# Optimization experiments

Hardware: AMD Instinct MI355X
Metric: run time of the kernel (lower is better)

Reference implementation:

```python
import jax, jax.numpy as jnp
import numpy as np

D_MODEL = 1024
H = 16
HEAD = D_MODEL // H  # 64


def setup_inputs() -> dict:
    key = jax.random.key(0)
    ks = jax.random.split(key, 10)
    B, S = 2, 2048
    x = jax.random.normal(ks[0], (B, S, D_MODEL), dtype=jnp.float32)
    y = jax.random.normal(ks[1], (B, S, D_MODEL), dtype=jnp.float32)
    mask = jnp.ones((B, S, S), dtype=jnp.float32)
    s = 1.0 / np.sqrt(D_MODEL)
    Wq = jax.random.normal(ks[2], (D_MODEL, D_MODEL), dtype=jnp.float32) * s
    Wk = jax.random.normal(ks[3], (D_MODEL, D_MODEL), dtype=jnp.float32) * s
    Wv = jax.random.normal(ks[4], (D_MODEL, D_MODEL), dtype=jnp.float32) * s
    Wo = jax.random.normal(ks[5], (D_MODEL, D_MODEL), dtype=jnp.float32) * s
    bq = jnp.zeros((D_MODEL,), jnp.float32)
    bk = jnp.zeros((D_MODEL,), jnp.float32)
    bv = jnp.zeros((D_MODEL,), jnp.float32)
    bo = jnp.zeros((D_MODEL,), jnp.float32)
    return {"x": x, "y": y, "mask": mask, "Wq": Wq, "bq": bq, "Wk": Wk,
            "bk": bk, "Wv": Wv, "bv": bv, "Wo": Wo, "bo": bo}


def reference(x, y, mask, Wq, bq, Wk, bk, Wv, bv, Wo, bo):
    # torch Linear: out = in @ W.T + b; here W stored as [out, in]
    B, Sq, D = x.shape
    Skv = y.shape[1]
    q = x @ Wq.T + bq  # [B, Sq, D]
    k = y @ Wk.T + bk  # [B, Skv, D]
    v = y @ Wv.T + bv
    # chunk(h, dim=-1) + cat(dim=0) == split feature dim into heads (head-major)
    q = q.reshape(B, Sq, H, HEAD)
    k = k.reshape(B, Skv, H, HEAD)
    v = v.reshape(B, Skv, H, HEAD)
    score = jnp.einsum('bqhd,bkhd->bhqk', q, k) / np.sqrt(HEAD)
    score = score + (1.0 - mask[:, None, :, :]) * -1e9
    attn = jax.nn.softmax(score, axis=-1)
    out = jnp.einsum('bhqk,bkhd->bqhd', attn, v).reshape(B, Sq, D)
    return out @ Wo.T + bo
```

## Files before the change

### kernel.cpp

```cpp
#include <hip/hip_runtime.h>
#include <cstdint>
#include <cstddef>

typedef __bf16 bf16x8 __attribute__((ext_vector_type(8)));
typedef float f32x4 __attribute__((ext_vector_type(4)));
typedef unsigned short u16;
typedef unsigned short u16x8 __attribute__((ext_vector_type(8)));
typedef unsigned int u32;

typedef __attribute__((address_space(1))) void gvoid_t;
typedef __attribute__((address_space(3))) void lvoid_t;

__device__ __forceinline__ void gld_lds16(const void* g, void* l) {
  __builtin_amdgcn_global_load_lds((gvoid_t*)g, (lvoid_t*)l, 16, 0, 0);
}

__device__ __forceinline__ u16 f2bf(float f) {
  u32 u = __float_as_uint(f);
  u += 0x7fffu + ((u >> 16) & 1u);
  return (u16)(u >> 16);
}
__device__ __forceinline__ u32 pack_rnd(float a, float b) {
  const u32 ua = __float_as_uint(a) + 0x8000u;
  const u32 ub = __float_as_uint(b) + 0x8000u;
  return __builtin_amdgcn_perm(ub, ua, 0x07060302u);
}
__device__ __forceinline__ bf16x8 ld_frag(const u16* p) {
  return __builtin_bit_cast(bf16x8, *(const uint4*)p);
}
__device__ __forceinline__ f32x4 mfma16(bf16x8 a, bf16x8 b, f32x4 c) {
  return __builtin_amdgcn_mfma_f32_16x16x32_bf16(a, b, c, 0, 0, 0);
}
__device__ __forceinline__ float ex2(float x) {
  return __builtin_amdgcn_exp2f(x);
}

#define D_MODEL 1024
#define SEQ     2048
#define NHEAD   16
#define QSC     0.1803368801f
#define MBIAS   (-1.4426950408e9f)

__global__ __launch_bounds__(256) void cvt_kernel(
    const float* __restrict__ x,  const float* __restrict__ y,
    const float* __restrict__ wq, const float* __restrict__ wk,
    const float* __restrict__ wv, const float* __restrict__ wo,
    u16* __restrict__ xb, u16* __restrict__ yb,
    u16* __restrict__ wqb, u16* __restrict__ wkb,
    u16* __restrict__ wvb, u16* __restrict__ wob) {
  const int t = blockIdx.y;
  const float* src;
  u16* dst;
  int n;
  float sc = 1.0f;
  if (t == 0)      { src = x;  dst = xb;  n = 4096 * 1024; }
  else if (t == 1) { src = y;  dst = yb;  n = 4096 * 1024; }
  else if (t == 2) { src = wq; dst = wqb; n = 1024 * 1024; sc = QSC; }
  else if (t == 3) { src = wk; dst = wkb; n = 1024 * 1024; }
  else if (t == 4) { src = wv; dst = wvb; n = 1024 * 1024; }
  else             { src = wo; dst = wob; n = 1024 * 1024; }
  const int i = (blockIdx.x * 256 + threadIdx.x) * 8;
  if (i >= n) return;
  const float4 a = *(const float4*)(src + i);
  const float4 b = *(const float4*)(src + i + 4);
  ushort4 lo, hi;
  lo.x = f2bf(a.x * sc); lo.y = f2bf(a.y * sc); lo.z = f2bf(a.z * sc); lo.w = f2bf(a.w * sc);
  hi.x = f2bf(b.x * sc); hi.y = f2bf(b.y * sc); hi.z = f2bf(b.z * sc); hi.w = f2bf(b.w * sc);
  *(ushort4*)(dst + i) = lo;
  *(ushort4*)(dst + i + 4) = hi;
}

__global__ __launch_bounds__(256) void maskC_kernel(
    const float* __restrict__ mask, u16* __restrict__ biasC) {
  const int i = (blockIdx.x * 256 + threadIdx.x) * 8;
  const float4 a = *(const float4*)(mask + i);
  const float4 b = *(const float4*)(mask + i + 4);
  ushort4 lo, hi;
  lo.x = f2bf(MBIAS - a.x * MBIAS); lo.y = f2bf(MBIAS - a.y * MBIAS);
  lo.z = f2bf(MBIAS - a.z * MBIAS); lo.w = f2bf(MBIAS - a.w * MBIAS);
  hi.x = f2bf(MBIAS - b.x * MBIAS); hi.y = f2bf(MBIAS - b.y * MBIAS);
  hi.z = f2bf(MBIAS - b.z * MBIAS); hi.w = f2bf(MBIAS - b.w * MBIAS);
  *(ushort4*)(biasC + i) = lo;
  *(ushort4*)(biasC + i + 4) = hi;
}

__global__ __launch_bounds__(256) void vT_kernel(
    const u16* __restrict__ vbuf, u16* __restrict__ vt) {
  const int st = blockIdx.x, h = blockIdx.y, b = blockIdx.z;
  const int tid = threadIdx.x;
  __shared__ u16 Lt[64 * 72];
  const int r = tid >> 2;
  const int cb = (tid & 3) * 16;
  const u16* ip = vbuf + ((size_t)(b * SEQ + st * 64 + r)) * D_MODEL + h * 64 + cb;
  uint4 a0 = *(const uint4*)ip;
  uint4 a1 = *(const uint4*)(ip + 8);
#pragma unroll
  for (int j = 0; j < 8; ++j) {
    Lt[(cb + j) * 72 + r]     = ((const u16*)&a0)[j];
    Lt[(cb + 8 + j) * 72 + r] = ((const u16*)&a1)[j];
  }
  __syncthreads();
  u16 v[16];
#pragma unroll
  for (int j = 0; j < 16; ++j) v[j] = Lt[r * 72 + cb + j];
  u16* op = vt + ((size_t)((b * NHEAD + h) * 64 + r)) * SEQ + st * 64 + cb;
  *(uint4*)op = *(const uint4*)v;
  *(uint4*)(op + 8) = *(const uint4*)(v + 8);
}

template <typename OT>
__device__ __forceinline__ void gemm_block_128(const u16* __restrict__ A,
                                               const u16* __restrict__ W,
                                               const float* __restrict__ bias,
                                               float bscale,
                                               OT* __restrict__ D,
                                               int mb, int nb) {
  __shared__ __align__(16) u16 Asl[128 * 64];
  __shared__ __align__(16) u16 Bsl[128 * 64];
  const int tid = threadIdx.x;
  const int w = tid >> 6, lane = tid & 63, quad = lane >> 4, l16 = lane & 15;
  const int wm = (w & 1) * 64, wn = (w >> 1) * 64;
  const int cidx = w * 64 + lane;

  f32x4 acc[4][4];
#pragma unroll
  for (int i = 0; i < 4; ++i)
#pragma unroll
    for (int j = 0; j < 4; ++j) acc[i][j] = f32x4{0.f, 0.f, 0.f, 0.f};

  for (int k0 = 0; k0 < 1024; k0 += 64) {
    __syncthreads();
#pragma unroll
    for (int t = 0; t < 4; ++t) {
      const int idx = t * 256 + cidx;
      const int row = idx >> 3;
      const int g = (idx & 7) ^ (row & 7);
      const size_t dst = (size_t)(t * 4 + w) * 1024;
      gld_lds16(A + (size_t)(mb * 128 + row) * 1024 + k0 + g * 8, (char*)Asl + dst);
      gld_lds16(W + (size_t)(nb * 128 + row) * 1024 + k0 + g * 8, (char*)Bsl + dst);
    }
    __syncthreads();

#pragma unroll
    for (int kk = 0; kk < 2; ++kk) {
      bf16x8 af[4], bfr[4];
#pragma unroll
      for (int i = 0; i < 4; ++i) {
        const int ar = wm + i * 16 + l16;
        const int br = wn + i * 16 + l16;
        af[i]  = ld_frag(Asl + ar * 64 + (((kk * 4 + quad) ^ (ar & 7)) * 8));
        bfr[i] = ld_frag(Bsl + br * 64 + (((kk * 4 + quad) ^ (br & 7)) * 8));
      }
#pragma unroll
      for (int i = 0; i < 4; ++i)
#pragma unroll
        for (int j = 0; j < 4; ++j) acc[i][j] = mfma16(af[i], bfr[j], acc[i][j]);
    }
  }

#pragma unroll
  for (int i = 0; i < 4; ++i)
#pragma unroll
    for (int j = 0; j < 4; ++j) {
      const int gn = nb * 128 + wn + j * 16 + l16;
      const float bv = bias[gn] * bscale;
#pragma unroll
      for (int r = 0; r < 4; ++r) {
        const int gm = mb * 128 + wm + i * 16 + quad * 4 + r;
        const float v = acc[i][j][r] + bv;
        if constexpr (sizeof(OT) == 2)
          D[(size_t)gm * 1024 + gn] = (OT)f2bf(v);
        else
          D[(size_t)gm * 1024 + gn] = (OT)v;
      }
    }
}

__global__ __launch_bounds__(256) void qkv_kernel(
    const u16* __restrict__ xb, const u16* __restrict__ yb,
    const u16* __restrict__ Wqb, const u16* __restrict__ Wkb, const u16* __restrict__ Wvb,
    const float* __restrict__ bq, const float* __restrict__ bk, const float* __restrict__ bv,
    u16* __restrict__ qb, u16* __restrict__ kb, u16* __restrict__ vb) {
  const int mat = blockIdx.y >> 3;
  const int nb = blockIdx.y & 7;
  const int mb = blockIdx.x;
  const u16 *A, *W;
  const float* bias;
  u16* D;
  float bscale = 1.0f;
  if (mat == 0)      { A = xb; W = Wqb; bias = bq; D = qb; bscale = QSC; }
  else if (mat == 1) { A = yb; W = Wkb; bias = bk; D = kb; }
  else               { A = yb; W = Wvb; bias = bv; D = vb; }
  gemm_block_128<u16>(A, W, bias, bscale, D, mb, nb);
}

__global__ __launch_bounds__(256) void oproj_kernel(
    const u16* __restrict__ ctx, const u16* __restrict__ Wob,
    const float* __restrict__ bo, float* __restrict__ out) {
  gemm_block_128<float>(ctx, Wob, bo, 1.0f, out, blockIdx.x, blockIdx.y);
}

__global__ __launch_bounds__(256) void attn_kernel(
    const u16* __restrict__ qb, const u16* __restrict__ kb,
    const u16* __restrict__ vt, const u16* __restrict__ biasC,
    u16* __restrict__ ctx) {
  const int h = blockIdx.x;
  const int qblk = blockIdx.y;
  const int b = blockIdx.z;
  const int tid = threadIdx.x, w = tid >> 6, lane = tid & 63;
  const int quad = lane >> 4, l16 = lane & 15;
  const int q0 = qblk * 128;

  __shared__ __align__(16) u16 Ks[64 * 64];
  __shared__ __align__(16) u16 Vs[64 * 64];
  __shared__ __align__(16) u16 Bs[128 * 64];
  __shared__ __align__(16) u16 Ps[4 * 32 * 64];

  const int qbase = w * 32;
  bf16x8 qf[2][2];
#pragma unroll
  for (int f = 0; f < 2; ++f) {
    const u16* qp = qb + (size_t)(b * SEQ + q0 + qbase + f * 16 + l16) * D_MODEL + h * 64;
    qf[f][0] = ld_frag(qp + quad * 8);
    qf[f][1] = ld_frag(qp + 32 + quad * 8);
  }
  bf16x8 onesf;
  {
    u16x8 t;
    const u16 ov = (l16 == 0) ? (u16)0x3F80 : (u16)0;
#pragma unroll
    for (int j = 0; j < 8; ++j) t[j] = ov;
    onesf = __builtin_bit_cast(bf16x8, t);
  }

  f32x4 O[2][4];
#pragma unroll
  for (int f = 0; f < 2; ++f)
#pragma unroll
    for (int dt = 0; dt < 4; ++dt) O[f][dt] = f32x4{0.f, 0.f, 0.f, 0.f};
  f32x4 O4[2] = {f32x4{0.f, 0.f, 0.f, 0.f}, f32x4{0.f, 0.f, 0.f, 0.f}};

  const int cidx = w * 64 + lane;
  u16* Pw = Ps + w * 2048;

  for (int kt = 0; kt < 32; ++kt) {
    const int kv0 = kt * 64;

    __syncthreads();
#pragma unroll
    for (int t = 0; t < 2; ++t) {
      const int idx = t * 256 + cidx;
      const int row = idx >> 3;
      const int g = (idx & 7) ^ (row & 7);
      const size_t dst = (size_t)(t * 4 + w) * 1024;
      gld_lds16(kb + (size_t)(b * SEQ + kv0 + row) * D_MODEL + h * 64 + g * 8,
                (char*)Ks + dst);
      gld_lds16(vt + ((size_t)((b * NHEAD + h) * 64 + row)) * SEQ + kv0 + g * 8,
                (char*)Vs + dst);
    }
#pragma unroll
    for (int t = 0; t < 4; ++t) {
      const int idx = t * 256 + cidx;
      const int row = idx >> 3;
      const int g = (idx & 7) ^ (row & 7);
      gld_lds16(biasC + (size_t)(b * SEQ + q0 + row) * SEQ + kv0 + g * 8,
                (char*)Bs + (size_t)(t * 4 + w) * 1024);
    }
    __syncthreads();

#pragma unroll
    for (int nt = 0; nt < 4; ++nt) {
      const int kvl = nt * 16 + l16;
      const bf16x8 kf0 = ld_frag(Ks + kvl * 64 + ((quad ^ (kvl & 7)) * 8));
      const bf16x8 kf1 = ld_frag(Ks + kvl * 64 + (((4 + quad) ^ (kvl & 7)) * 8));
#pragma unroll
      for (int f = 0; f < 2; ++f) {
        const int br = qbase + f * 16 + l16;
        const int ck = nt * 2 + (quad >> 1);
        const uint2 bw = *(const uint2*)(Bs + br * 64 + ((ck ^ (br & 7)) * 8) + (quad & 1) * 4);
        f32x4 z;
        z[0] = __uint_as_float(bw.x << 16);
        z[1] = __uint_as_float(bw.x & 0xffff0000u);
        z[2] = __uint_as_float(bw.y << 16);
        z[3] = __uint_as_float(bw.y & 0xffff0000u);
        z = mfma16(kf0, qf[f][0], z);
        z = mfma16(kf1, qf[f][1], z);
        uint2 pv;
        pv.x = pack_rnd(ex2(z[0]), ex2(z[1]));
        pv.y = pack_rnd(ex2(z[2]), ex2(z[3]));
        const int pr = f * 16 + l16;
        *(uint2*)(Pw + pr * 64 + ((ck ^ (pr & 7)) * 8) + (quad & 1) * 4) = pv;
      }
    }

    bf16x8 pf[2][2];
#pragma unroll
    for (int f = 0; f < 2; ++f) {
      const int pr = f * 16 + l16;
      pf[f][0] = ld_frag(Pw + pr * 64 + ((quad ^ (pr & 7)) * 8));
      pf[f][1] = ld_frag(Pw + pr * 64 + (((4 + quad) ^ (pr & 7)) * 8));
    }
#pragma unroll
    for (int dt = 0; dt < 4; ++dt) {
      const int vr = dt * 16 + l16;
      const bf16x8 vf0 = ld_frag(Vs + vr * 64 + ((quad ^ (vr & 7)) * 8));
      const bf16x8 vf1 = ld_frag(Vs + vr * 64 + (((4 + quad) ^ (vr & 7)) * 8));
#pragma unroll
      for (int f = 0; f < 2; ++f) {
        O[f][dt] = mfma16(pf[f][0], vf0, O[f][dt]);
        O[f][dt] = mfma16(pf[f][1], vf1, O[f][dt]);
      }
    }
#pragma unroll
    for (int f = 0; f < 2; ++f) {
      O4[f] = mfma16(pf[f][0], onesf, O4[f]);
      O4[f] = mfma16(pf[f][1], onesf, O4[f]);
    }
  }

  float inv[2][4];
#pragma unroll
  for (int f = 0; f < 2; ++f)
#pragma unroll
    for (int r = 0; r < 4; ++r)
      inv[f][r] = 1.0f / __shfl(O4[f][r], lane & 48, 64);

#pragma unroll
  for (int f = 0; f < 2; ++f)
#pragma unroll
    for (int dt = 0; dt < 4; ++dt)
#pragma unroll
      for (int r = 0; r < 4; ++r) {
        const int gq = b * SEQ + q0 + qbase + f * 16 + quad * 4 + r;
        const int gd = h * 64 + dt * 16 + l16;
        ctx[(size_t)gq * D_MODEL + gd] = f2bf(O[f][dt][r] * inv[f][r]);
      }
}

extern "C" void kernel_launch(void* const* d_in, const int* in_sizes, int n_in,
                              void* d_out, int out_size, void* d_ws, size_t ws_size,
                              hipStream_t stream) {
  (void)in_sizes; (void)n_in; (void)out_size; (void)ws_size;
  const float* x    = (const float*)d_in[0];
  const float* y    = (const float*)d_in[1];
  const float* mask = (const float*)d_in[2];
  const float* Wq   = (const float*)d_in[3];
  const float* bq   = (const float*)d_in[4];
  const float* Wk   = (const float*)d_in[5];
  const float* bk   = (const float*)d_in[6];
  const float* Wv   = (const float*)d_in[7];
  const float* bv   = (const float*)d_in[8];
  const float* Wo   = (const float*)d_in[9];
  const float* bo   = (const float*)d_in[10];
  float* out = (float*)d_out;

  const size_t M4 = (size_t)4096 * 1024;
  const size_t M1 = (size_t)1024 * 1024;
  u16* qbuf  = (u16*)d_ws;
  u16* kbuf  = qbuf + M4;
  u16* vt    = kbuf + M4;
  u16* vbuf  = vt + M4;
  u16* cbuf  = vbuf;
  u16* wob   = vbuf + M4;
  u16* xb    = wob + M1;
  u16* yb    = xb + M4;
  u16* wqb   = yb + M4;
  u16* wkb   = wqb + M1;
  u16* wvb   = wkb + M1;
  u16* biasC = xb;

  cvt_kernel<<<dim3(2048, 6, 1), 256, 0, stream>>>(x, y, Wq, Wk, Wv, Wo,
                                                   xb, yb, wqb, wkb, wvb, wob);
  qkv_kernel<<<dim3(32, 24, 1), 256, 0, stream>>>(xb, yb, wqb, wkb, wvb,
                                                  bq, bk, bv, qbuf, kbuf, vbuf);
  vT_kernel<<<dim3(32, NHEAD, 2), 256, 0, stream>>>(vbuf, vt);
  maskC_kernel<<<dim3(4096, 1, 1), 256, 0, stream>>>(mask, biasC);
  attn_kernel<<<dim3(NHEAD, 16, 2), 256, 0, stream>>>(qbuf, kbuf, vt, biasC, cbuf);
  oproj_kernel<<<dim3(32, 8, 1), 256, 0, stream>>>(cbuf, wob, bo, out);
}
```

Before: 269.8 us.

## Fuse V transpose into QKV GEMM epilogue and merge mask/Wo prep

The V projection now writes its output transposed per head directly from the GEMM epilogue, staging the tile through a swizzled shared-memory buffer. This removes the separate vT kernel and the intermediate V buffer round trip. The mask-bias and Wo conversions are merged into one prep kernel, which cuts one launch. P packing in attention now uses the library float2-to-bf16 round-to-nearest-even conversion instead of the hand-rolled round-half-up perm, which may cost a few extra instructions in the hot loop.

```diff
diff --git a/kernel.cpp b/kernel.cpp
--- a/kernel.cpp
+++ b/kernel.cpp
@@ -1,4 +1,5 @@
 #include <hip/hip_runtime.h>
+#include <hip/hip_bf16.h>
 #include <cstdint>
 #include <cstddef>
 
@@ -20,10 +21,11 @@
   u += 0x7fffu + ((u >> 16) & 1u);
   return (u16)(u >> 16);
 }
-__device__ __forceinline__ u32 pack_rnd(float a, float b) {
-  const u32 ua = __float_as_uint(a) + 0x8000u;
-  const u32 ub = __float_as_uint(b) + 0x8000u;
-  return __builtin_amdgcn_perm(ub, ua, 0x07060302u);
+__device__ __forceinline__ u32 pack2(float a, float b) {
+  __hip_bfloat162 h = __float22bfloat162_rn(float2{a, b});
+  u32 r;
+  __builtin_memcpy(&r, &h, 4);
+  return r;
 }
 __device__ __forceinline__ bf16x8 ld_frag(const u16* p) {
   return __builtin_bit_cast(bf16x8, *(const uint4*)p);
@@ -44,10 +46,9 @@
 __global__ __launch_bounds__(256) void cvt_kernel(
     const float* __restrict__ x,  const float* __restrict__ y,
     const float* __restrict__ wq, const float* __restrict__ wk,
-    const float* __restrict__ wv, const float* __restrict__ wo,
+    const float* __restrict__ wv,
     u16* __restrict__ xb, u16* __restrict__ yb,
-    u16* __restrict__ wqb, u16* __restrict__ wkb,
-    u16* __restrict__ wvb, u16* __restrict__ wob) {
+    u16* __restrict__ wqb, u16* __restrict__ wkb, u16* __restrict__ wvb) {
   const int t = blockIdx.y;
   const float* src;
   u16* dst;
@@ -57,8 +58,7 @@
   else if (t == 1) { src = y;  dst = yb;  n = 4096 * 1024; }
   else if (t == 2) { src = wq; dst = wqb; n = 1024 * 1024; sc = QSC; }
   else if (t == 3) { src = wk; dst = wkb; n = 1024 * 1024; }
-  else if (t == 4) { src = wv; dst = wvb; n = 1024 * 1024; }
-  else             { src = wo; dst = wob; n = 1024 * 1024; }
+  else             { src = wv; dst = wvb; n = 1024 * 1024; }
   const int i = (blockIdx.x * 256 + threadIdx.x) * 8;
   if (i >= n) return;
   const float4 a = *(const float4*)(src + i);
@@ -70,53 +70,43 @@
   *(ushort4*)(dst + i + 4) = hi;
 }
 
-__global__ __launch_bounds__(256) void maskC_kernel(
-    const float* __restrict__ mask, u16* __restrict__ biasC) {
-  const int i = (blockIdx.x * 256 + threadIdx.x) * 8;
-  const float4 a = *(const float4*)(mask + i);
-  const float4 b = *(const float4*)(mask + i + 4);
-  ushort4 lo, hi;
-  lo.x = f2bf(MBIAS - a.x * MBIAS); lo.y = f2bf(MBIAS - a.y * MBIAS);
-  lo.z = f2bf(MBIAS - a.z * MBIAS); lo.w = f2bf(MBIAS - a.w * MBIAS);
-  hi.x = f2bf(MBIAS - b.x * MBIAS); hi.y = f2bf(MBIAS - b.y * MBIAS);
-  hi.z = f2bf(MBIAS - b.z * MBIAS); hi.w = f2bf(MBIAS - b.w * MBIAS);
-  *(ushort4*)(biasC + i) = lo;
-  *(ushort4*)(biasC + i + 4) = hi;
-}
-
-__global__ __launch_bounds__(256) void vT_kernel(
-    const u16* __restrict__ vbuf, u16* __restrict__ vt) {
-  const int st = blockIdx.x, h = blockIdx.y, b = blockIdx.z;
-  const int tid = threadIdx.x;
-  __shared__ u16 Lt[64 * 72];
-  const int r = tid >> 2;
-  const int cb = (tid & 3) * 16;
-  const u16* ip = vbuf + ((size_t)(b * SEQ + st * 64 + r)) * D_MODEL + h * 64 + cb;
-  uint4 a0 = *(const uint4*)ip;
-  uint4 a1 = *(const uint4*)(ip + 8);
-#pragma unroll
-  for (int j = 0; j < 8; ++j) {
-    Lt[(cb + j) * 72 + r]     = ((const u16*)&a0)[j];
-    Lt[(cb + 8 + j) * 72 + r] = ((const u16*)&a1)[j];
-  }
-  __syncthreads();
-  u16 v[16];
-#pragma unroll
-  for (int j = 0; j < 16; ++j) v[j] = Lt[r * 72 + cb + j];
-  u16* op = vt + ((size_t)((b * NHEAD + h) * 64 + r)) * SEQ + st * 64 + cb;
-  *(uint4*)op = *(const uint4*)v;
-  *(uint4*)(op + 8) = *(const uint4*)(v + 8);
-}
-
-template <typename OT>
+__global__ __launch_bounds__(256) void prep_kernel(
+    const float* __restrict__ mask, const float* __restrict__ wo,
+    u16* __restrict__ biasC, u16* __restrict__ wob) {
+  const int bid = blockIdx.x;
+  if (bid < 4096) {
+    const int i = (bid * 256 + threadIdx.x) * 8;
+    const float4 a = *(const float4*)(mask + i);
+    const float4 b = *(const float4*)(mask + i + 4);
+    ushort4 lo, hi;
+    lo.x = f2bf(MBIAS - a.x * MBIAS); lo.y = f2bf(MBIAS - a.y * MBIAS);
+    lo.z = f2bf(MBIAS - a.z * MBIAS); lo.w = f2bf(MBIAS - a.w * MBIAS);
+    hi.x = f2bf(MBIAS - b.x * MBIAS); hi.y = f2bf(MBIAS - b.y * MBIAS);
+    hi.z = f2bf(MBIAS - b.z * MBIAS); hi.w = f2bf(MBIAS - b.w * MBIAS);
+    *(ushort4*)(biasC + i) = lo;
+    *(ushort4*)(biasC + i + 4) = hi;
+  } else {
+    const int i = ((bid - 4096) * 256 + threadIdx.x) * 8;
+    const float4 a = *(const float4*)(wo + i);
+    const float4 b = *(const float4*)(wo + i + 4);
+    ushort4 lo, hi;
+    lo.x = f2bf(a.x); lo.y = f2bf(a.y); lo.z = f2bf(a.z); lo.w = f2bf(a.w);
+    hi.x = f2bf(b.x); hi.y = f2bf(b.y); hi.z = f2bf(b.z); hi.w = f2bf(b.w);
+    *(ushort4*)(wob + i) = lo;
+    *(ushort4*)(wob + i + 4) = hi;
+  }
+}
+
+template <int MODE, typename OT>
 __device__ __forceinline__ void gemm_block_128(const u16* __restrict__ A,
                                                const u16* __restrict__ W,
                                                const float* __restrict__ bias,
                                                float bscale,
                                                OT* __restrict__ D,
                                                int mb, int nb) {
-  __shared__ __align__(16) u16 Asl[128 * 64];
-  __shared__ __align__(16) u16 Bsl[128 * 64];
+  __shared__ __align__(16) u16 S[16384];
+  u16* Asl = S;
+  u16* Bsl = S + 8192;
   const int tid = threadIdx.x;
   const int w = tid >> 6, lane = tid & 63, quad = lane >> 4, l16 = lane & 15;
   const int wm = (w & 1) * 64, wn = (w >> 1) * 64;
@@ -158,46 +148,66 @@
     }
   }
 
-#pragma unroll
-  for (int i = 0; i < 4; ++i)
-#pragma unroll
-    for (int j = 0; j < 4; ++j) {
-      const int gn = nb * 128 + wn + j * 16 + l16;
-      const float bv = bias[gn] * bscale;
-#pragma unroll
-      for (int r = 0; r < 4; ++r) {
-        const int gm = mb * 128 + wm + i * 16 + quad * 4 + r;
-        const float v = acc[i][j][r] + bv;
-        if constexpr (sizeof(OT) == 2)
-          D[(size_t)gm * 1024 + gn] = (OT)f2bf(v);
-        else
-          D[(size_t)gm * 1024 + gn] = (OT)v;
-      }
-    }
+  if constexpr (MODE == 2) {
+    __syncthreads();
+#pragma unroll
+    for (int i = 0; i < 4; ++i)
+#pragma unroll
+      for (int j = 0; j < 4; ++j) {
+        const int dl = wn + j * 16 + l16;
+        const float bv = bias[nb * 128 + dl];
+        const int sx = (wm + i * 16 + quad * 4) ^ ((dl & 15) << 3);
+        uint2 pv;
+        pv.x = (u32)f2bf(acc[i][j][0] + bv) | ((u32)f2bf(acc[i][j][1] + bv) << 16);
+        pv.y = (u32)f2bf(acc[i][j][2] + bv) | ((u32)f2bf(acc[i][j][3] + bv) << 16);
+        *(uint2*)(S + dl * 128 + sx) = pv;
+      }
+    __syncthreads();
+    const int dl = tid >> 1, half = tid & 1;
+    const int bb = mb >> 4, s0 = (mb & 15) * 128;
+    u16* vrow = (u16*)D + (size_t)(bb * 1024 + nb * 128 + dl) * SEQ + s0 + half * 64;
+#pragma unroll
+    for (int c = 0; c < 8; ++c) {
+      const int pc = (half * 8 + c) ^ (dl & 15);
+      *(uint4*)(vrow + c * 8) = *(const uint4*)(S + dl * 128 + pc * 8);
+    }
+  } else {
+#pragma unroll
+    for (int i = 0; i < 4; ++i)
+#pragma unroll
+      for (int j = 0; j < 4; ++j) {
+        const int gn = nb * 128 + wn + j * 16 + l16;
+        const float bv = bias[gn] * bscale;
+#pragma unroll
+        for (int r = 0; r < 4; ++r) {
+          const int gm = mb * 128 + wm + i * 16 + quad * 4 + r;
+          const float v = acc[i][j][r] + bv;
+          if constexpr (sizeof(OT) == 2)
+            D[(size_t)gm * 1024 + gn] = (OT)f2bf(v);
+          else
+            D[(size_t)gm * 1024 + gn] = (OT)v;
+        }
+      }
+  }
 }
 
 __global__ __launch_bounds__(256) void qkv_kernel(
     const u16* __restrict__ xb, const u16* __restrict__ yb,
     const u16* __restrict__ Wqb, const u16* __restrict__ Wkb, const u16* __restrict__ Wvb,
     const float* __restrict__ bq, const float* __restrict__ bk, const float* __restrict__ bv,
-    u16* __restrict__ qb, u16* __restrict__ kb, u16* __restrict__ vb) {
+    u16* __restrict__ qb, u16* __restrict__ kb, u16* __restrict__ vt) {
   const int mat = blockIdx.y >> 3;
   const int nb = blockIdx.y & 7;
   const int mb = blockIdx.x;
-  const u16 *A, *W;
-  const float* bias;
-  u16* D;
-  float bscale = 1.0f;
-  if (mat == 0)      { A = xb; W = Wqb; bias = bq; D = qb; bscale = QSC; }
-  else if (mat == 1) { A = yb; W = Wkb; bias = bk; D = kb; }
-  else               { A = yb; W = Wvb; bias = bv; D = vb; }
-  gemm_block_128<u16>(A, W, bias, bscale, D, mb, nb);
+  if (mat == 0)      gemm_block_128<0, u16>(xb, Wqb, bq, QSC,  qb, mb, nb);
+  else if (mat == 1) gemm_block_128<0, u16>(yb, Wkb, bk, 1.0f, kb, mb, nb);
+  else               gemm_block_128<2, u16>(yb, Wvb, bv, 1.0f, vt, mb, nb);
 }
 
 __global__ __launch_bounds__(256) void oproj_kernel(
     const u16* __restrict__ ctx, const u16* __restrict__ Wob,
     const float* __restrict__ bo, float* __restrict__ out) {
-  gemm_block_128<float>(ctx, Wob, bo, 1.0f, out, blockIdx.x, blockIdx.y);
+  gemm_block_128<1, float>(ctx, Wob, bo, 1.0f, out, blockIdx.x, blockIdx.y);
 }
 
 __global__ __launch_bounds__(256) void attn_kernel(
@@ -286,8 +296,8 @@
         z = mfma16(kf0, qf[f][0], z);
         z = mfma16(kf1, qf[f][1], z);
         uint2 pv;
-        pv.x = pack_rnd(ex2(z[0]), ex2(z[1]));
-        pv.y = pack_rnd(ex2(z[2]), ex2(z[3]));
+        pv.x = pack2(ex2(z[0]), ex2(z[1]));
+        pv.y = pack2(ex2(z[2]), ex2(z[3]));
         const int pr = f * 16 + l16;
         *(uint2*)(Pw + pr * 64 + ((ck ^ (pr & 7)) * 8) + (quad & 1) * 4) = pv;
       }
@@ -359,9 +369,8 @@
   u16* qbuf  = (u16*)d_ws;
   u16* kbuf  = qbuf + M4;
   u16* vt    = kbuf + M4;
-  u16* vbuf  = vt + M4;
-  u16* cbuf  = vbuf;
-  u16* wob   = vbuf + M4;
+  u16* cbuf  = vt + M4;
+  u16* wob   = cbuf + M4;
   u16* xb    = wob + M1;
   u16* yb    = xb + M4;
   u16* wqb   = yb + M4;
@@ -369,12 +378,11 @@
   u16* wvb   = wkb + M1;
   u16* biasC = xb;
 
-  cvt_kernel<<<dim3(2048, 6, 1), 256, 0, stream>>>(x, y, Wq, Wk, Wv, Wo,
-                                                   xb, yb, wqb, wkb, wvb, wob);
+  cvt_kernel<<<dim3(2048, 5, 1), 256, 0, stream>>>(x, y, Wq, Wk, Wv,
+                                                   xb, yb, wqb, wkb, wvb);
   qkv_kernel<<<dim3(32, 24, 1), 256, 0, stream>>>(xb, yb, wqb, wkb, wvb,
-                                                  bq, bk, bv, qbuf, kbuf, vbuf);
-  vT_kernel<<<dim3(32, NHEAD, 2), 256, 0, stream>>>(vbuf, vt);
-  maskC_kernel<<<dim3(4096, 1, 1), 256, 0, stream>>>(mask, biasC);
+                                                  bq, bk, bv, qbuf, kbuf, vt);
+  prep_kernel<<<dim3(4608, 1, 1), 256, 0, stream>>>(mask, Wo, biasC, wob);
   attn_kernel<<<dim3(NHEAD, 16, 2), 256, 0, stream>>>(qbuf, kbuf, vt, biasC, cbuf);
   oproj_kernel<<<dim3(32, 8, 1), 256, 0, stream>>>(cbuf, wob, bo, out);
 }
```

Measured after the change: 270.4 us. Within noise of the previous version (+0.2%).
